# Kernel optimization log

Measured on AMD Instinct MI355X. Metric: run time of the kernel, lower is better.

Reference implementation:

```python
import jax, jax.numpy as jnp
import numpy as np

HIDDEN = 32
WINDOW = 128
ALPHA = 2.5
T_LEN = 524288


def setup_inputs() -> dict:
    key = jax.random.key(0)
    ks = jax.random.split(key, 9)
    H = HIDDEN
    s = 1.0 / np.sqrt(H)
    u = lambda k, shape: jax.random.uniform(k, shape, jnp.float32, -s, s)
    return {
        "x": jax.random.normal(ks[0], (1, T_LEN, 1), jnp.float32),
        "Wih": u(ks[1], (3 * H, 2)),
        "Whh": u(ks[2], (3 * H, H)),
        "bih": u(ks[3], (3 * H,)),
        "bhh": u(ks[4], (3 * H,)),
        "Wv": u(ks[5], (H, 1)),
        "bv": u(ks[6], (1,)),
        "Ws": u(ks[7], (H, 1)),
        "bs": u(ks[8], (1,)),
    }


def _spike_mask(x1):
    """Vectorized replacement of the per-timestep Python loop.
    mask[t] True iff |x[t] - (2x[t-1]-x[t-2])| > alpha*(sqrt(mean(x[max(0,t-W):t]^2))+1e-8).
    Uses a prefix sum of x^2 for the sliding-window mean. mask[0]=mask[1]=True."""
    T = x1.shape[0]
    cs = jnp.concatenate([jnp.zeros((1,), x1.dtype), jnp.cumsum(x1 * x1)])  # [T+1]
    t = jnp.arange(T)
    ws = jnp.maximum(0, t - WINDOW)
    cnt = jnp.maximum(t - ws, 1).astype(x1.dtype)
    rms = jnp.sqrt(jnp.maximum(cs[t] - cs[ws], 0.0) / cnt) + 1e-8
    pred = 2.0 * jnp.roll(x1, 1) - jnp.roll(x1, 2)  # garbage at t<2, overwritten below
    err = jnp.abs(x1 - pred)
    mask = err > (ALPHA * rms)
    return mask.at[:2].set(True)


def _gru_cell(inp, h, Wih, Whh, bih, bhh):
    H = h.shape[0]
    gi = Wih @ inp + bih  # [3H]
    gh = Whh @ h + bhh    # [3H]
    r = jax.nn.sigmoid(gi[:H] + gh[:H])
    z = jax.nn.sigmoid(gi[H:2 * H] + gh[H:2 * H])
    n = jnp.tanh(gi[2 * H:] + r * gh[2 * H:])
    return (1.0 - z) * n + z * h


def reference(x, Wih, Whh, bih, bhh, Wv, bv, Ws, bs):
    x1 = x[0, :, 0]                       # [T]
    T = x1.shape[0]
    mask = _spike_mask(x1)                # [T] bool (non-differentiable, as in torch detach)
    tf = jnp.arange(T, dtype=x1.dtype)

    # GRU state is only updated at event steps (equivalent to running the GRU over the
    # compacted event sequence); between events the held state is used for linear
    # extrapolation val + slope * (t - t_event)/window.
    def step(carry, inp):
        h, last_t = carry
        xt, m, t = inp
        delta = (t - last_t) / float(WINDOW)
        h_new = _gru_cell(jnp.stack([xt, delta]), h, Wih, Whh, bih, bhh)
        h = jnp.where(m, h_new, h)
        last_t = jnp.where(m, t, last_t)
        dt = (t - last_t) / float(WINDOW)  # 0 at event steps
        out = (h @ Wv + bv) + (h @ Ws + bs) * dt  # [1]
        return (h, last_t), out[0]

    init = (jnp.zeros((HIDDEN,), x1.dtype), jnp.zeros((), x1.dtype))
    _, outs = jax.lax.scan(step, init, (x1, mask, tf))
    output = outs.reshape(1, T, 1)
    N = jnp.sum(mask.astype(jnp.int32))
    return output, N, mask
```

## Files before the change

kernel.cpp:

```cpp
#include <hip/hip_runtime.h>
#include <stdint.h>

#define T_LEN 524288
#define SEG 8
#define WARM 8
#define EPC (SEG + WARM + 1)
#define CHAINS 16
#define GSP (CHAINS * SEG)
#define CBLK 1536

typedef short short8 __attribute__((ext_vector_type(8)));
typedef float f4 __attribute__((ext_vector_type(4)));
#define KEEPA(v) asm volatile("" : "+v"(v))

static const size_t OFF_MASK = 0;
static const size_t OFF_CNT  = T_LEN;
static const size_t OFF_BOFF = T_LEN + 2048;
static const size_t OFF_N    = T_LEN + 4096;
static const size_t OFF_SPK  = T_LEN + 8192;

__device__ __forceinline__ short bfr(float f) {
    uint32_t u = __float_as_uint(f);
    u = (u + 0x7fffu + ((u >> 16) & 1u)) >> 16;
    return (short)u;
}

__global__ __launch_bounds__(256) void k_mask(const float* __restrict__ x,
                                              uint8_t* __restrict__ mask,
                                              float* __restrict__ out, int out_size,
                                              int* __restrict__ cnt)
{
    __shared__ float tile[1154];
    __shared__ int tot;
    const int bs = blockIdx.x * 1024;
    const int tid = threadIdx.x;
    if (tid == 0) tot = 0;
    for (int j = tid; j < 1154; j += 256) {
        int g = bs - 130 + j;
        tile[j] = (g >= 0) ? x[g] : 0.f;
    }
    __syncthreads();
    const int loc = tid * 4;
    float s = 0.f;
    #pragma unroll 16
    for (int m = 0; m < 128; ++m) { float v = tile[loc + 2 + m]; s = fmaf(v, v, s); }
    uchar4 mv; float4 mf; int msum = 0;
    uint8_t* mp = &mv.x; float* fp = &mf.x;
    #pragma unroll
    for (int it = 0; it < 4; ++it) {
        int t = bs + loc + it;
        int c = t < 128 ? (t < 1 ? 1 : t) : 128;
        float rms = sqrtf(fmaxf(s, 0.f) / (float)c) + 1e-8f;
        float xt = tile[loc + 130 + it];
        float pr = 2.f * tile[loc + 129 + it] - tile[loc + 128 + it];
        bool m = (t < 2) || (fabsf(xt - pr) > 2.5f * rms);
        mp[it] = m ? 1 : 0; fp[it] = m ? 1.f : 0.f; msum += m ? 1 : 0;
        float a = tile[loc + 130 + it], d = tile[loc + 2 + it];
        s = fmaf(a, a, s) - d * d;
    }
    *(uchar4*)(mask + bs + loc) = mv;
    int oi = T_LEN + 1 + bs + loc;
    if (oi + 3 < out_size) *(float4*)(out + oi) = mf;
    for (int d = 32; d; d >>= 1) msum += __shfl_down(msum, d, 64);
    if ((tid & 63) == 0) atomicAdd(&tot, msum);
    __syncthreads();
    if (tid == 0) cnt[blockIdx.x] = tot;
}

__global__ __launch_bounds__(512) void k_scan(const int* __restrict__ cnt,
                                              int* __restrict__ boff,
                                              int* __restrict__ nspk,
                                              float* __restrict__ out, int out_size)
{
    __shared__ int buf[2][512];
    int t = threadIdx.x;
    int v = cnt[t];
    buf[0][t] = v;
    __syncthreads();
    int src = 0;
    for (int d = 1; d < 512; d <<= 1) {
        int nv = buf[src][t] + (t >= d ? buf[src][t - d] : 0);
        buf[src ^ 1][t] = nv;
        __syncthreads();
        src ^= 1;
    }
    boff[t] = buf[src][t] - v;
    if (t == 511) {
        *nspk = buf[src][511];
        if (T_LEN < out_size) out[T_LEN] = (float)buf[src][511];
    }
}

__global__ __launch_bounds__(256) void k_scatter(const uint8_t* __restrict__ mask,
                                                 const int* __restrict__ boff,
                                                 int* __restrict__ spk)
{
    __shared__ int wtot[4];
    const int tid = threadIdx.x, b = blockIdx.x;
    const int base = b * 1024 + tid * 4;
    uchar4 mv = *(const uchar4*)(mask + base);
    int m0 = mv.x, m1 = mv.y, m2 = mv.z, m3 = mv.w;
    int e1 = m0, e2 = m0 + m1, e3 = m0 + m1 + m2, tsum = e3 + m3;
    int lane = tid & 63, w = tid >> 6;
    int incl = tsum;
    for (int d = 1; d < 64; d <<= 1) {
        int u = __shfl_up(incl, d, 64);
        if (lane >= d) incl += u;
    }
    if (lane == 63) wtot[w] = incl;
    __syncthreads();
    int woff = 0;
    for (int i = 0; i < w; i++) woff += wtot[i];
    int texcl = woff + incl - tsum;
    int g = boff[b] + texcl;
    int e[4] = {0, e1, e2, e3};
    int m[4] = {m0, m1, m2, m3};
    #pragma unroll
    for (int k = 0; k < 4; k++) {
        if (m[k]) spk[g + e[k]] = base + k;
    }
}

__global__ __attribute__((amdgpu_waves_per_eu(2)))
__launch_bounds__(64)
void k_chain(const float* __restrict__ Whh,
             const float* __restrict__ Wih,
             const float* __restrict__ bih,
             const float* __restrict__ bhh,
             const int* __restrict__ spk,
             const float* __restrict__ x,
             const int* __restrict__ nspk,
             const float* __restrict__ Wv,
             const float* __restrict__ bv,
             const float* __restrict__ Wsc,
             const float* __restrict__ bs,
             float* __restrict__ out)
{
    __shared__ float2   st[CHAINS * EPC];
    __shared__ unsigned hx[CHAINS * 20];
    __shared__ float    ab[2 * GSP];

    const int lane = threadIdx.x;
    const int m = lane & 15;
    const int quad = lane >> 4;
    const int N = *nspk;

    short8 A1[6], A2[6], A3;
    #pragma unroll
    for (int t = 0; t < 6; ++t) {
        union { short s[8]; short8 v; } u1, u2;
        int rowg = 16 * t + m;
        #pragma unroll
        for (int j = 0; j < 8; ++j) {
            int k = 8 * quad + j;
            u1.s[j] = bfr(Whh[rowg * 32 + k]);
            float a2v = 0.f;
            if (k == 0) a2v = Wih[rowg * 2];
            else if (k == 1) a2v = Wih[rowg * 2 + 1];
            else if (k == 2) a2v = (rowg < 64) ? (bih[rowg] + bhh[rowg]) : bih[rowg];
            u2.s[j] = bfr(a2v);
        }
        A1[t] = u1.v; A2[t] = u2.v;
    }
    {
        union { short s[8]; short8 v; } u3;
        #pragma unroll
        for (int j = 0; j < 8; ++j) {
            int k = 8 * quad + j;
            float v = (m == 0) ? Wv[k] : (m == 1) ? Wsc[k] : 0.f;
            u3.s[j] = bfr(v);
        }
        A3 = u3.v;
    }
    #pragma unroll
    for (int t = 0; t < 6; ++t) { KEEPA(A1[t]); KEEPA(A2[t]); }
    KEEPA(A3);

    float bn0[4], bn1[4];
    #pragma unroll
    for (int e = 0; e < 4; ++e) {
        int r0 = quad * 4 + e;
        bn0[e] = bhh[64 + r0];  bn1[e] = bhh[80 + r0];
    }
    const float bv0 = bv[0], bs0 = bs[0];

    for (int g0 = blockIdx.x; g0 * GSP < N; g0 += CBLK) {
        const int base0 = g0 * GSP;
        for (int e = lane; e < CHAINS * EPC; e += 64) {
            int n = e / EPC, j = e - n * EPC;
            int s = base0 + n * SEG - (WARM + 1) + j;
            s = min(max(s, 0), N - 1);
            int t = spk[s];
            st[e] = make_float2((float)t, x[t]);
        }
        __builtin_amdgcn_wave_barrier();

        float h0[4], h1[4];
        #pragma unroll
        for (int e = 0; e < 4; ++e) { h0[e] = 0.f; h1[e] = 0.f; }
        short8 B1 = (short8)0;
        float tprev = st[m * EPC].x;

        for (int j = 0; j < SEG + WARM; ++j) {
            float2 cur = st[m * EPC + j + 1];
            float xt = cur.y;
            float d = (cur.x - tprev) * 0.0078125f;
            tprev = cur.x;

            unsigned p0 = (__float_as_uint(d) & 0xFFFF0000u) | (__float_as_uint(xt) >> 16);
            unsigned p1 = 0x00003F80u;
            p0 = (quad == 0) ? p0 : 0u;
            p1 = (quad == 0) ? p1 : 0u;
            union { unsigned u[4]; short8 v; } b2u;
            b2u.u[0] = p0; b2u.u[1] = p1; b2u.u[2] = 0u; b2u.u[3] = 0u;
            short8 B2 = b2u.v;

            f4 z4 = {0.f, 0.f, 0.f, 0.f};
            f4 Drz[4], Dh0, Dh1, Di0, Di1;
            f4 tmp0 = __builtin_amdgcn_mfma_f32_16x16x32_bf16(A2[0], B2, z4, 0, 0, 0);
            f4 tmp1 = __builtin_amdgcn_mfma_f32_16x16x32_bf16(A2[1], B2, z4, 0, 0, 0);
            f4 tmp2 = __builtin_amdgcn_mfma_f32_16x16x32_bf16(A2[2], B2, z4, 0, 0, 0);
            f4 tmp3 = __builtin_amdgcn_mfma_f32_16x16x32_bf16(A2[3], B2, z4, 0, 0, 0);
            Di0 = __builtin_amdgcn_mfma_f32_16x16x32_bf16(A2[4], B2, z4, 0, 0, 0);
            Di1 = __builtin_amdgcn_mfma_f32_16x16x32_bf16(A2[5], B2, z4, 0, 0, 0);
            Drz[0] = __builtin_amdgcn_mfma_f32_16x16x32_bf16(A1[0], B1, tmp0, 0, 0, 0);
            Drz[1] = __builtin_amdgcn_mfma_f32_16x16x32_bf16(A1[1], B1, tmp1, 0, 0, 0);
            Drz[2] = __builtin_amdgcn_mfma_f32_16x16x32_bf16(A1[2], B1, tmp2, 0, 0, 0);
            Drz[3] = __builtin_amdgcn_mfma_f32_16x16x32_bf16(A1[3], B1, tmp3, 0, 0, 0);
            Dh0 = __builtin_amdgcn_mfma_f32_16x16x32_bf16(A1[4], B1, z4, 0, 0, 0);
            Dh1 = __builtin_amdgcn_mfma_f32_16x16x32_bf16(A1[5], B1, z4, 0, 0, 0);

            #pragma unroll
            for (int e = 0; e < 4; ++e) {
                float r0 = __builtin_amdgcn_rcpf(1.f + __builtin_amdgcn_exp2f(-1.44269504089f * Drz[0][e]));
                float r1 = __builtin_amdgcn_rcpf(1.f + __builtin_amdgcn_exp2f(-1.44269504089f * Drz[1][e]));
                float zz0 = __builtin_amdgcn_rcpf(1.f + __builtin_amdgcn_exp2f(-1.44269504089f * Drz[2][e]));
                float zz1 = __builtin_amdgcn_rcpf(1.f + __builtin_amdgcn_exp2f(-1.44269504089f * Drz[3][e]));
                float np0 = fmaf(r0, Dh0[e] + bn0[e], Di0[e]);
                float np1 = fmaf(r1, Dh1[e] + bn1[e], Di1[e]);
                float en0 = __builtin_amdgcn_exp2f(2.88539008178f * np0);
                float en1 = __builtin_amdgcn_exp2f(2.88539008178f * np1);
                float n0 = fmaf(-2.f, __builtin_amdgcn_rcpf(1.f + en0), 1.f);
                float n1 = fmaf(-2.f, __builtin_amdgcn_rcpf(1.f + en1), 1.f);
                h0[e] = fmaf(zz0, h0[e] - n0, n0);
                h1[e] = fmaf(zz1, h1[e] - n1, n1);
            }

            unsigned q0 = (__float_as_uint(h0[1]) & 0xFFFF0000u) | (__float_as_uint(h0[0]) >> 16);
            unsigned q1 = (__float_as_uint(h0[3]) & 0xFFFF0000u) | (__float_as_uint(h0[2]) >> 16);
            unsigned q2 = (__float_as_uint(h1[1]) & 0xFFFF0000u) | (__float_as_uint(h1[0]) >> 16);
            unsigned q3 = (__float_as_uint(h1[3]) & 0xFFFF0000u) | (__float_as_uint(h1[2]) >> 16);
            *(uint2*)&hx[m * 20 + 2 * quad]     = make_uint2(q0, q1);
            *(uint2*)&hx[m * 20 + 8 + 2 * quad] = make_uint2(q2, q3);
            __builtin_amdgcn_wave_barrier();
            union { uint4 u; short8 v; } bu;
            bu.u = *(const uint4*)&hx[m * 20 + 4 * quad];
            B1 = bu.v;

            if (j >= WARM) {
                f4 Dab = __builtin_amdgcn_mfma_f32_16x16x32_bf16(A3, B1, z4, 0, 0, 0);
                if (quad == 0) {
                    int sg = base0 + m * SEG + (j - WARM);
                    if (sg < N)
                        *(float2*)&ab[2 * (m * SEG + j - WARM)] =
                            make_float2(Dab[0] + bv0, Dab[1] + bs0);
                }
            }
        }
        __builtin_amdgcn_wave_barrier();

        const int nid = base0 + GSP;
        const int tN = (nid >= N) ? T_LEN : spk[nid];
        #pragma unroll
        for (int h = 0; h < 2; ++h) {
            int sl = lane + 64 * h;
            int sg = base0 + sl;
            if (sg < N) {
                int n = sl >> 3, jj = sl & 7;
                float ts = st[n * EPC + (WARM + 1) + jj].x;
                int tnext;
                if (sg + 1 >= N) tnext = T_LEN;
                else if (sl + 1 < GSP) {
                    int n2 = (sl + 1) >> 3, j2 = (sl + 1) & 7;
                    tnext = (int)st[n2 * EPC + (WARM + 1) + j2].x;
                } else tnext = tN;
                float2 abv = *(const float2*)&ab[2 * sl];
                int tsi = (int)ts;
                for (int t = tsi; t < tnext; ++t)
                    out[t] = fmaf(abv.y, (float)(t - tsi) * 0.0078125f, abv.x);
            }
        }
        __builtin_amdgcn_wave_barrier();
    }
}

extern "C" void kernel_launch(void* const* d_in, const int* in_sizes, int n_in,
                              void* d_out, int out_size, void* d_ws, size_t ws_size,
                              hipStream_t stream)
{
    const float* x   = (const float*)d_in[0];
    const float* Wih = (const float*)d_in[1];
    const float* Whh = (const float*)d_in[2];
    const float* bih = (const float*)d_in[3];
    const float* bhh = (const float*)d_in[4];
    const float* Wv  = (const float*)d_in[5];
    const float* bv  = (const float*)d_in[6];
    const float* Wsc = (const float*)d_in[7];
    const float* bs  = (const float*)d_in[8];
    float* out = (float*)d_out;

    char* ws = (char*)d_ws;
    uint8_t* mask = (uint8_t*)(ws + OFF_MASK);
    int* cnt  = (int*)(ws + OFF_CNT);
    int* boff = (int*)(ws + OFF_BOFF);
    int* nspk = (int*)(ws + OFF_N);
    int* spk  = (int*)(ws + OFF_SPK);

    k_mask<<<512, 256, 0, stream>>>(x, mask, out, out_size, cnt);
    k_scan<<<1, 512, 0, stream>>>(cnt, boff, nspk, out, out_size);
    k_scatter<<<512, 256, 0, stream>>>(mask, boff, spk);
    k_chain<<<CBLK, 64, 0, stream>>>(Whh, Wih, bih, bhh, spk, x, nspk,
                                     Wv, bv, Wsc, bs, out);
}
```

Measured before the change: 106.1 us.

## Fuse scan into scatter, shorten chain segments, swap LDS exchange for bpermute

Drops the separate single-block scan kernel. Each scatter block now sums its predecessor counts directly, and the last block writes N. The GRU chain kernel halves the segment length (SEG 8→4) and raises the grid (CBLK) and waves-per-EU, which exposes more parallel chains. It exchanges the hidden state across lanes with ds_bpermute instead of an LDS store/load plus barrier, and prefetches the next event. The changes trade more warm-up recompute per output (warm 8 vs seg 4) and redundant prefix sums in the scatter for fewer kernel launches and shorter serial chains.

```diff
diff --git a/kernel.cpp b/kernel.cpp
--- a/kernel.cpp
+++ b/kernel.cpp
@@ -2,12 +2,12 @@
 #include <stdint.h>
 
 #define T_LEN 524288
-#define SEG 8
+#define SEG 4
 #define WARM 8
 #define EPC (SEG + WARM + 1)
 #define CHAINS 16
 #define GSP (CHAINS * SEG)
-#define CBLK 1536
+#define CBLK 2560
 
 typedef short short8 __attribute__((ext_vector_type(8)));
 typedef float f4 __attribute__((ext_vector_type(4)));
@@ -15,7 +15,6 @@
 
 static const size_t OFF_MASK = 0;
 static const size_t OFF_CNT  = T_LEN;
-static const size_t OFF_BOFF = T_LEN + 2048;
 static const size_t OFF_N    = T_LEN + 4096;
 static const size_t OFF_SPK  = T_LEN + 8192;
 
@@ -23,6 +22,9 @@
     uint32_t u = __float_as_uint(f);
     u = (u + 0x7fffu + ((u >> 16) & 1u)) >> 16;
     return (short)u;
+}
+__device__ __forceinline__ unsigned pk(float hi, float lo) {
+    return (((unsigned)(unsigned short)bfr(hi)) << 16) | (unsigned short)bfr(lo);
 }
 
 __global__ __launch_bounds__(256) void k_mask(const float* __restrict__ x,
@@ -67,61 +69,56 @@
     if (tid == 0) cnt[blockIdx.x] = tot;
 }
 
-__global__ __launch_bounds__(512) void k_scan(const int* __restrict__ cnt,
-                                              int* __restrict__ boff,
-                                              int* __restrict__ nspk,
-                                              float* __restrict__ out, int out_size)
-{
-    __shared__ int buf[2][512];
-    int t = threadIdx.x;
-    int v = cnt[t];
-    buf[0][t] = v;
-    __syncthreads();
-    int src = 0;
-    for (int d = 1; d < 512; d <<= 1) {
-        int nv = buf[src][t] + (t >= d ? buf[src][t - d] : 0);
-        buf[src ^ 1][t] = nv;
-        __syncthreads();
-        src ^= 1;
-    }
-    boff[t] = buf[src][t] - v;
-    if (t == 511) {
-        *nspk = buf[src][511];
-        if (T_LEN < out_size) out[T_LEN] = (float)buf[src][511];
-    }
-}
-
 __global__ __launch_bounds__(256) void k_scatter(const uint8_t* __restrict__ mask,
-                                                 const int* __restrict__ boff,
-                                                 int* __restrict__ spk)
+                                                 const int* __restrict__ cnt,
+                                                 int* __restrict__ spk,
+                                                 int* __restrict__ nspk,
+                                                 float* __restrict__ out)
 {
     __shared__ int wtot[4];
+    __shared__ int sh_base;
     const int tid = threadIdx.x, b = blockIdx.x;
+    const int lane = tid & 63, w = tid >> 6;
     const int base = b * 1024 + tid * 4;
     uchar4 mv = *(const uchar4*)(mask + base);
     int m0 = mv.x, m1 = mv.y, m2 = mv.z, m3 = mv.w;
     int e1 = m0, e2 = m0 + m1, e3 = m0 + m1 + m2, tsum = e3 + m3;
-    int lane = tid & 63, w = tid >> 6;
     int incl = tsum;
     for (int d = 1; d < 64; d <<= 1) {
         int u = __shfl_up(incl, d, 64);
         if (lane >= d) incl += u;
     }
     if (lane == 63) wtot[w] = incl;
+
+    if (w == 0) {
+        int pre = 0;
+        #pragma unroll
+        for (int k8 = 0; k8 < 8; ++k8) {
+            int idx = k8 * 64 + lane;
+            pre += (idx < b) ? cnt[idx] : 0;
+        }
+        for (int d = 32; d; d >>= 1) pre += __shfl_down(pre, d, 64);
+        if (lane == 0) sh_base = pre;
+    }
     __syncthreads();
     int woff = 0;
     for (int i = 0; i < w; i++) woff += wtot[i];
     int texcl = woff + incl - tsum;
-    int g = boff[b] + texcl;
+    int g = sh_base + texcl;
     int e[4] = {0, e1, e2, e3};
     int m[4] = {m0, m1, m2, m3};
     #pragma unroll
     for (int k = 0; k < 4; k++) {
         if (m[k]) spk[g + e[k]] = base + k;
     }
-}
-
-__global__ __attribute__((amdgpu_waves_per_eu(2)))
+    if (b == 511 && tid == 0) {
+        int N = sh_base + wtot[0] + wtot[1] + wtot[2] + wtot[3];
+        *nspk = N;
+        out[T_LEN] = (float)N;
+    }
+}
+
+__global__ __attribute__((amdgpu_waves_per_eu(3)))
 __launch_bounds__(64)
 void k_chain(const float* __restrict__ Whh,
              const float* __restrict__ Wih,
@@ -136,9 +133,8 @@
              const float* __restrict__ bs,
              float* __restrict__ out)
 {
-    __shared__ float2   st[CHAINS * EPC];
-    __shared__ unsigned hx[CHAINS * 20];
-    __shared__ float    ab[2 * GSP];
+    __shared__ float2 st[CHAINS * EPC];
+    __shared__ float  ab[2 * GSP];
 
     const int lane = threadIdx.x;
     const int m = lane & 15;
@@ -184,6 +180,10 @@
     }
     const float bv0 = bv[0], bs0 = bs[0];
 
+    const int aA = ((((2 * quad) & 3) * 16 + m) << 2);
+    const int aB = ((((2 * quad + 1) & 3) * 16 + m) << 2);
+    const bool ql = (quad < 2);
+
     for (int g0 = blockIdx.x; g0 * GSP < N; g0 += CBLK) {
         const int base0 = g0 * GSP;
         for (int e = lane; e < CHAINS * EPC; e += 64) {
@@ -200,9 +200,10 @@
         for (int e = 0; e < 4; ++e) { h0[e] = 0.f; h1[e] = 0.f; }
         short8 B1 = (short8)0;
         float tprev = st[m * EPC].x;
+        float2 cur = st[m * EPC + 1];
 
         for (int j = 0; j < SEG + WARM; ++j) {
-            float2 cur = st[m * EPC + j + 1];
+            float2 nxt = st[m * EPC + min(j + 2, EPC - 1)];
             float xt = cur.y;
             float d = (cur.x - tprev) * 0.0078125f;
             tprev = cur.x;
@@ -216,26 +217,25 @@
             short8 B2 = b2u.v;
 
             f4 z4 = {0.f, 0.f, 0.f, 0.f};
-            f4 Drz[4], Dh0, Dh1, Di0, Di1;
-            f4 tmp0 = __builtin_amdgcn_mfma_f32_16x16x32_bf16(A2[0], B2, z4, 0, 0, 0);
-            f4 tmp1 = __builtin_amdgcn_mfma_f32_16x16x32_bf16(A2[1], B2, z4, 0, 0, 0);
-            f4 tmp2 = __builtin_amdgcn_mfma_f32_16x16x32_bf16(A2[2], B2, z4, 0, 0, 0);
-            f4 tmp3 = __builtin_amdgcn_mfma_f32_16x16x32_bf16(A2[3], B2, z4, 0, 0, 0);
-            Di0 = __builtin_amdgcn_mfma_f32_16x16x32_bf16(A2[4], B2, z4, 0, 0, 0);
-            Di1 = __builtin_amdgcn_mfma_f32_16x16x32_bf16(A2[5], B2, z4, 0, 0, 0);
-            Drz[0] = __builtin_amdgcn_mfma_f32_16x16x32_bf16(A1[0], B1, tmp0, 0, 0, 0);
-            Drz[1] = __builtin_amdgcn_mfma_f32_16x16x32_bf16(A1[1], B1, tmp1, 0, 0, 0);
-            Drz[2] = __builtin_amdgcn_mfma_f32_16x16x32_bf16(A1[2], B1, tmp2, 0, 0, 0);
-            Drz[3] = __builtin_amdgcn_mfma_f32_16x16x32_bf16(A1[3], B1, tmp3, 0, 0, 0);
-            Dh0 = __builtin_amdgcn_mfma_f32_16x16x32_bf16(A1[4], B1, z4, 0, 0, 0);
-            Dh1 = __builtin_amdgcn_mfma_f32_16x16x32_bf16(A1[5], B1, z4, 0, 0, 0);
+            f4 t0 = __builtin_amdgcn_mfma_f32_16x16x32_bf16(A2[0], B2, z4, 0, 0, 0);
+            f4 t1 = __builtin_amdgcn_mfma_f32_16x16x32_bf16(A2[1], B2, z4, 0, 0, 0);
+            f4 t2 = __builtin_amdgcn_mfma_f32_16x16x32_bf16(A2[2], B2, z4, 0, 0, 0);
+            f4 t3 = __builtin_amdgcn_mfma_f32_16x16x32_bf16(A2[3], B2, z4, 0, 0, 0);
+            f4 Di0 = __builtin_amdgcn_mfma_f32_16x16x32_bf16(A2[4], B2, z4, 0, 0, 0);
+            f4 Di1 = __builtin_amdgcn_mfma_f32_16x16x32_bf16(A2[5], B2, z4, 0, 0, 0);
+            f4 Dr0 = __builtin_amdgcn_mfma_f32_16x16x32_bf16(A1[0], B1, t0, 0, 0, 0);
+            f4 Dr1 = __builtin_amdgcn_mfma_f32_16x16x32_bf16(A1[1], B1, t1, 0, 0, 0);
+            f4 Dz0 = __builtin_amdgcn_mfma_f32_16x16x32_bf16(A1[2], B1, t2, 0, 0, 0);
+            f4 Dz1 = __builtin_amdgcn_mfma_f32_16x16x32_bf16(A1[3], B1, t3, 0, 0, 0);
+            f4 Dh0 = __builtin_amdgcn_mfma_f32_16x16x32_bf16(A1[4], B1, z4, 0, 0, 0);
+            f4 Dh1 = __builtin_amdgcn_mfma_f32_16x16x32_bf16(A1[5], B1, z4, 0, 0, 0);
 
             #pragma unroll
             for (int e = 0; e < 4; ++e) {
-                float r0 = __builtin_amdgcn_rcpf(1.f + __builtin_amdgcn_exp2f(-1.44269504089f * Drz[0][e]));
-                float r1 = __builtin_amdgcn_rcpf(1.f + __builtin_amdgcn_exp2f(-1.44269504089f * Drz[1][e]));
-                float zz0 = __builtin_amdgcn_rcpf(1.f + __builtin_amdgcn_exp2f(-1.44269504089f * Drz[2][e]));
-                float zz1 = __builtin_amdgcn_rcpf(1.f + __builtin_amdgcn_exp2f(-1.44269504089f * Drz[3][e]));
+                float r0 = __builtin_amdgcn_rcpf(1.f + __builtin_amdgcn_exp2f(-1.44269504089f * Dr0[e]));
+                float r1 = __builtin_amdgcn_rcpf(1.f + __builtin_amdgcn_exp2f(-1.44269504089f * Dr1[e]));
+                float zz0 = __builtin_amdgcn_rcpf(1.f + __builtin_amdgcn_exp2f(-1.44269504089f * Dz0[e]));
+                float zz1 = __builtin_amdgcn_rcpf(1.f + __builtin_amdgcn_exp2f(-1.44269504089f * Dz1[e]));
                 float np0 = fmaf(r0, Dh0[e] + bn0[e], Di0[e]);
                 float np1 = fmaf(r1, Dh1[e] + bn1[e], Di1[e]);
                 float en0 = __builtin_amdgcn_exp2f(2.88539008178f * np0);
@@ -246,45 +246,47 @@
                 h1[e] = fmaf(zz1, h1[e] - n1, n1);
             }
 
-            unsigned q0 = (__float_as_uint(h0[1]) & 0xFFFF0000u) | (__float_as_uint(h0[0]) >> 16);
-            unsigned q1 = (__float_as_uint(h0[3]) & 0xFFFF0000u) | (__float_as_uint(h0[2]) >> 16);
-            unsigned q2 = (__float_as_uint(h1[1]) & 0xFFFF0000u) | (__float_as_uint(h1[0]) >> 16);
-            unsigned q3 = (__float_as_uint(h1[3]) & 0xFFFF0000u) | (__float_as_uint(h1[2]) >> 16);
-            *(uint2*)&hx[m * 20 + 2 * quad]     = make_uint2(q0, q1);
-            *(uint2*)&hx[m * 20 + 8 + 2 * quad] = make_uint2(q2, q3);
-            __builtin_amdgcn_wave_barrier();
-            union { uint4 u; short8 v; } bu;
-            bu.u = *(const uint4*)&hx[m * 20 + 4 * quad];
+            unsigned q0 = pk(h0[1], h0[0]);
+            unsigned q1 = pk(h0[3], h0[2]);
+            unsigned q2 = pk(h1[1], h1[0]);
+            unsigned q3 = pk(h1[3], h1[2]);
+            unsigned tA0 = __builtin_amdgcn_ds_bpermute(aA, (int)q0);
+            unsigned tA1 = __builtin_amdgcn_ds_bpermute(aA, (int)q1);
+            unsigned tA2 = __builtin_amdgcn_ds_bpermute(aA, (int)q2);
+            unsigned tA3 = __builtin_amdgcn_ds_bpermute(aA, (int)q3);
+            unsigned tB0 = __builtin_amdgcn_ds_bpermute(aB, (int)q0);
+            unsigned tB1 = __builtin_amdgcn_ds_bpermute(aB, (int)q1);
+            unsigned tB2 = __builtin_amdgcn_ds_bpermute(aB, (int)q2);
+            unsigned tB3 = __builtin_amdgcn_ds_bpermute(aB, (int)q3);
+            union { unsigned u[4]; short8 v; } bu;
+            bu.u[0] = ql ? tA0 : tA2;
+            bu.u[1] = ql ? tA1 : tA3;
+            bu.u[2] = ql ? tB0 : tB2;
+            bu.u[3] = ql ? tB1 : tB3;
             B1 = bu.v;
 
             if (j >= WARM) {
                 f4 Dab = __builtin_amdgcn_mfma_f32_16x16x32_bf16(A3, B1, z4, 0, 0, 0);
-                if (quad == 0) {
-                    int sg = base0 + m * SEG + (j - WARM);
-                    if (sg < N)
-                        *(float2*)&ab[2 * (m * SEG + j - WARM)] =
-                            make_float2(Dab[0] + bv0, Dab[1] + bs0);
-                }
+                int sl = m * SEG + (j - WARM);
+                if (quad == 0 && base0 + sl < N)
+                    *(float2*)&ab[2 * sl] = make_float2(Dab[0] + bv0, Dab[1] + bs0);
             }
+            cur = nxt;
         }
         __builtin_amdgcn_wave_barrier();
 
-        const int nid = base0 + GSP;
-        const int tN = (nid >= N) ? T_LEN : spk[nid];
-        #pragma unroll
-        for (int h = 0; h < 2; ++h) {
-            int sl = lane + 64 * h;
-            int sg = base0 + sl;
+        {
+            int sg = base0 + lane;
             if (sg < N) {
-                int n = sl >> 3, jj = sl & 7;
+                int n = lane >> 2, jj = lane & 3;
                 float ts = st[n * EPC + (WARM + 1) + jj].x;
                 int tnext;
                 if (sg + 1 >= N) tnext = T_LEN;
-                else if (sl + 1 < GSP) {
-                    int n2 = (sl + 1) >> 3, j2 = (sl + 1) & 7;
+                else if (lane < 63) {
+                    int n2 = (lane + 1) >> 2, j2 = (lane + 1) & 3;
                     tnext = (int)st[n2 * EPC + (WARM + 1) + j2].x;
-                } else tnext = tN;
-                float2 abv = *(const float2*)&ab[2 * sl];
+                } else tnext = spk[base0 + GSP];
+                float2 abv = *(const float2*)&ab[2 * lane];
                 int tsi = (int)ts;
                 for (int t = tsi; t < tnext; ++t)
                     out[t] = fmaf(abv.y, (float)(t - tsi) * 0.0078125f, abv.x);
@@ -312,13 +314,11 @@
     char* ws = (char*)d_ws;
     uint8_t* mask = (uint8_t*)(ws + OFF_MASK);
     int* cnt  = (int*)(ws + OFF_CNT);
-    int* boff = (int*)(ws + OFF_BOFF);
     int* nspk = (int*)(ws + OFF_N);
     int* spk  = (int*)(ws + OFF_SPK);
 
     k_mask<<<512, 256, 0, stream>>>(x, mask, out, out_size, cnt);
-    k_scan<<<1, 512, 0, stream>>>(cnt, boff, nspk, out, out_size);
-    k_scatter<<<512, 256, 0, stream>>>(mask, boff, spk);
+    k_scatter<<<512, 256, 0, stream>>>(mask, cnt, spk, nspk, out);
     k_chain<<<CBLK, 64, 0, stream>>>(Whh, Wih, bih, bhh, spk, x, nspk,
                                      Wv, bv, Wsc, bs, out);
 }
```

Measured after the change: 110.0 us. 1.04x slower.
